# Kernel optimization log

Hardware: AMD Instinct MI355X
Metric: run time of the kernel (lower is better)

The kernel has to match this reference:

```python
import jax, jax.numpy as jnp
import numpy as np

B, N, D, NH, L, DFF = 2, 2048, 256, 8, 4, 1024
DH = D // NH
FACTOR = 0.5 / float(np.sqrt(DH))  # == 1/sqrt(4*DH), matches q/k feature dim 4*d_head
EPS = 1e-5


def _ln(x, g, b):
    m = x.mean(-1, keepdims=True)
    v = ((x - m) ** 2).mean(-1, keepdims=True)
    return (x - m) * jax.lax.rsqrt(v + EPS) * g + b


def setup_inputs() -> dict:
    key = jax.random.key(0)
    ks = jax.random.split(key, 16)
    s = 0.05
    r = lambda i, shape: jax.random.normal(ks[i], shape, dtype=jnp.float32)
    return {
        "H": r(0, (B, N, D)),
        "V": r(1, (B, N, 3, D)),
        "D_batch": r(2, (B, N, N)),
        "rbf_feat": r(3, (L, B, 1, N, N)),
        "H_mask": jnp.ones((B, N), dtype=bool),
        "ln1_g": jnp.ones((L, D)), "ln1_b": jnp.zeros((L, D)),
        "ln2_g": jnp.ones((L, D)), "ln2_b": jnp.zeros((L, D)),
        "Wq": r(4, (L, D, 4 * D)) * s, "bq": jnp.zeros((L, 4 * D)),
        "Wk": r(5, (L, D, 4 * D)) * s, "bk": jnp.zeros((L, 4 * D)),
        "Wv": r(6, (L, D, D)) * s, "bv": jnp.zeros((L, D)),
        "Wvv": r(7, (L, D, D)) * s,
        "Wo": r(8, (L, D, D)) * s, "bo": jnp.zeros((L, D)),
        "Wvo": r(9, (L, D, D)) * s,
        "Wlv": r(10, (L, D, 2 * D)) * s,
        "W1": r(11, (L, 2 * D, DFF)) * s, "b1": jnp.zeros((L, DFF)),
        "W2": r(12, (L, DFF, 2 * D)) * s, "b2": jnp.zeros((L, 2 * D)),
    }


def _stack_forward(H, V, D_batch, rbf_feat, H_mask, ln1_g, ln1_b, ln2_g, ln2_b,
                   Wq, bq, Wk, bk, Wv, bv, Wvv, Wo, bo, Wvo, Wlv, W1, b1, W2, b2):
    b, n = H.shape[:2]
    mask = H_mask[:, None, None, :]       # [B,1,1,N] masks key columns
    base_bias = D_batch[:, None]          # [B,1,N,N]

    def step(carry, xs):
        H, V = carry
        (rbf, g1, be1, g2, be2, wq, bq_, wk, bk_, wv, bv_, wvv,
         wo, bo_, wvo, wlv, w1, b1_, w2, b2_) = xs
        # --- self-attention sublayer (pre-LN on scalar stream only) ---
        Hn = _ln(H, g1, be1)
        Hq = (Hn @ wq + bq_).reshape(b, n, NH, 4 * DH)
        Hk = (Hn @ wk + bk_).reshape(b, n, NH, 4 * DH)
        Hv = (Hn @ wv + bv_).reshape(b, n, NH, DH)
        Vv = (V @ wvv).reshape(b, n, 3, NH, DH)
        Vv = jnp.swapaxes(Vv, 2, 3).reshape(b, n, NH, 3 * DH)
        V_attn = jnp.concatenate([Hv, Vv], axis=-1)        # [B,N,H,4*DH]
        bias = jnp.where(mask, rbf + base_bias, -jnp.inf)  # [B,1,N,N]
        scores = jnp.einsum('bnhd,bmhd->bhnm', Hq, Hk) * FACTOR + bias
        attn = jax.nn.softmax(scores, axis=-1)
        res = jnp.einsum('bhnm,bmhd->bnhd', attn, V_attn)  # [B,N,H,4*DH]
        H_res = res[..., :DH].reshape(b, n, D)
        V_res = jnp.swapaxes(res[..., DH:].reshape(b, n, NH, 3, DH), 2, 3).reshape(b, n, 3, D)
        H = H + (H_res @ wo + bo_)
        V = V + V_res @ wvo
        # --- GVP FFN sublayer (pre-LN on scalar stream only) ---
        Hn = _ln(H, g2, be2)
        Vp = V @ wlv                                       # [B,N,3,2D]
        V1, V2 = Vp[..., :D], Vp[..., D:]
        scaler = jnp.concatenate([Hn, jnp.linalg.norm(V1, axis=-2)], axis=-1)
        sc = jax.nn.silu(scaler @ w1 + b1_) @ w2 + b2_
        H = H + sc[..., :D]
        V = V + sc[..., D:][..., None, :] * V2             # vector_act='none'
        return (H, V), None

    xs = (rbf_feat, ln1_g, ln1_b, ln2_g, ln2_b, Wq, bq, Wk, bk, Wv, bv, Wvv,
          Wo, bo, Wvo, Wlv, W1, b1, W2, b2)
    (H, V), _ = jax.lax.scan(step, (H, V), xs)
    return H, V


def reference(H, V, D_batch, rbf_feat, H_mask, ln1_g, ln1_b, ln2_g, ln2_b,
              Wq, bq, Wk, bk, Wv, bv, Wvv, Wo, bo, Wvo, Wlv, W1, b1, W2, b2):
    return _stack_forward(H, V, D_batch, rbf_feat, H_mask, ln1_g, ln1_b, ln2_g, ln2_b,
                          Wq, bq, Wk, bk, Wv, bv, Wvv, Wo, bo, Wvo, Wlv, W1, b1, W2, b2)
```

## Files before the change

### kernel.cpp

```cpp
#include <hip/hip_runtime.h>
#include <math.h>

static constexpr int B_  = 2;
static constexpr int N_  = 2048;
static constexpr int D_  = 256;
static constexpr int NH_ = 8;
static constexpr int L_  = 4;
static constexpr int DH_ = 32;
static constexpr int DQ_ = 128;
static constexpr float FACTOR_ = 0.08838834764831845f;
static constexpr float LOG2E_  = 1.4426950408889634f;
static constexpr float EPS_ = 1e-5f;

typedef short    short8   __attribute__((ext_vector_type(8)));
typedef unsigned short us4 __attribute__((ext_vector_type(4)));
typedef unsigned short us8 __attribute__((ext_vector_type(8)));
typedef float    f32x4    __attribute__((ext_vector_type(4)));
typedef unsigned short us;

__device__ __forceinline__ us f2b(float f) {
  unsigned u = __float_as_uint(f);
  unsigned r = u + 0x7FFF + ((u >> 16) & 1);
  return (us)(r >> 16);
}
__device__ __forceinline__ float b2f(us u) {
  return __uint_as_float(((unsigned)u) << 16);
}
__device__ __forceinline__ float e2(float x) {
  return __builtin_amdgcn_exp2f(x);
}
__device__ __forceinline__ void gl_lds16(const void* g, void* l) {
  __builtin_amdgcn_global_load_lds(
      (const __attribute__((address_space(1))) void*)g,
      (__attribute__((address_space(3))) void*)l, 16, 0, 0);
}

__global__ __launch_bounds__(256) void ln_kernel(const float* __restrict__ X,
    const float* __restrict__ g, const float* __restrict__ b,
    us* __restrict__ Y) {
  __shared__ float r1[256], r2[256];
  int row = blockIdx.x, tid = threadIdx.x;
  float x = X[(size_t)row * D_ + tid];
  r1[tid] = x; r2[tid] = x * x;
  __syncthreads();
  for (int s = 128; s > 0; s >>= 1) {
    if (tid < s) { r1[tid] += r1[tid + s]; r2[tid] += r2[tid + s]; }
    __syncthreads();
  }
  float mean = r1[0] * (1.0f / D_);
  float var  = r2[0] * (1.0f / D_) - mean * mean;
  float inv  = rsqrtf(var + EPS_);
  Y[(size_t)row * D_ + tid] = f2b((x - mean) * inv * g[tid] + b[tid]);
}

__global__ __launch_bounds__(256) void conv_bf16(const float* __restrict__ X,
    us* __restrict__ Y) {
  size_t i = ((size_t)blockIdx.x * 256 + threadIdx.x) * 4;
  float4 v = *(const float4*)&X[i];
  us4 o = { f2b(v.x), f2b(v.y), f2b(v.z), f2b(v.w) };
  *(us4*)&Y[i] = o;
}

__global__ __launch_bounds__(256) void biascomb(const float* __restrict__ R,
    const float* __restrict__ Dq, us* __restrict__ Out) {
  size_t i = ((size_t)blockIdx.x * 256 + threadIdx.x) * 8;
  float4 r0 = *(const float4*)&R[i];
  float4 r1 = *(const float4*)&R[i + 4];
  float4 d0 = *(const float4*)&Dq[i];
  float4 d1 = *(const float4*)&Dq[i + 4];
  us8 o = { f2b((r0.x + d0.x) * LOG2E_), f2b((r0.y + d0.y) * LOG2E_),
            f2b((r0.z + d0.z) * LOG2E_), f2b((r0.w + d0.w) * LOG2E_),
            f2b((r1.x + d1.x) * LOG2E_), f2b((r1.y + d1.y) * LOG2E_),
            f2b((r1.z + d1.z) * LOG2E_), f2b((r1.w + d1.w) * LOG2E_) };
  *(us8*)&Out[i] = o;
}

struct WConvDesc {
  const float* src[9];
  unsigned dst[9];
  int K[9];
  int N[9];
  int start[10];
};
__global__ __launch_bounds__(256) void wconv_kernel(WConvDesc d, us* __restrict__ Wb) {
  __shared__ float T[64][65];
  int bid = blockIdx.x, tid = threadIdx.x;
  int j = 0;
  #pragma unroll
  for (int q = 0; q < 8; q++) if (bid >= d.start[q + 1]) j = q + 1;
  int t = bid - d.start[j];
  int K = d.K[j], N = d.N[j];
  int tpr = N >> 6;
  int tk = t / tpr, tn = t - tk * tpr;
  const float* src = d.src[j];
  us* dst = Wb + d.dst[j];
  #pragma unroll
  for (int i = 0; i < 4; i++) {
    int r = i * 16 + (tid >> 4), c = (tid & 15) * 4;
    *(float4*)&T[r][c] = *(const float4*)&src[(size_t)(tk * 64 + r) * N + tn * 64 + c];
  }
  __syncthreads();
  #pragma unroll
  for (int i = 0; i < 4; i++) {
    int n = i * 16 + (tid >> 4), k = (tid & 15) * 4;
    us4 o = { f2b(T[k][n]), f2b(T[k + 1][n]), f2b(T[k + 2][n]), f2b(T[k + 3][n]) };
    *(us4*)&dst[(size_t)(tn * 64 + n) * K + tk * 64 + k] = o;
  }
}

template<int BM, int BN, int BIAS, int ACC, int SILU, int WF, int WB, int QKV>
__global__ __launch_bounds__(256, 2) void gemm_v2(const us* __restrict__ A,
    const us* __restrict__ Wt, const float* __restrict__ bias,
    const float* __restrict__ bias2, const float* __restrict__ bias3,
    float* __restrict__ Cf, us* __restrict__ Cb,
    int M, int K, int Nc, float oscale) {
  constexpr int NFM = BM / 32, NFN = BN / 32;
  constexpr int WSM = NFM * 16, WSN = NFN * 16;
  constexpr int NLA = BM / 32, NLB = BN / 32;
  __shared__ us As[2][BM * 64];
  __shared__ us Bs[2][BN * 64];
  const int tid = threadIdx.x;
  const int w = tid >> 6, l = tid & 63;
  const int lx = l & 15, ly = l >> 4;
  const int wr = w >> 1, wc = w & 1;
  const int bn = blockIdx.x, bm = blockIdx.y;
  const int swz = (lx & 7) << 4;
  const char* Ag = (const char*)A + (size_t)(bm * BM) * K * 2;
  const char* Bg = (const char*)Wt + (size_t)(bn * BN) * K * 2;
  const size_t rowb = (size_t)K * 2;

  #define GSTAGE(buf, k0)                                                     \
    do {                                                                      \
      _Pragma("unroll")                                                       \
      for (int j = 0; j < NLA; j++) {                                         \
        int o = j * 4096 + tid * 16;                                          \
        int r = o >> 7, cb = o & 127;                                         \
        int sc = cb ^ ((r & 7) << 4);                                         \
        gl_lds16(Ag + (size_t)r * rowb + (size_t)(k0) * 2 + sc,               \
                 &As[buf][(j * 4096 + w * 1024) >> 1]);                       \
      }                                                                       \
      _Pragma("unroll")                                                       \
      for (int j = 0; j < NLB; j++) {                                         \
        int o = j * 4096 + tid * 16;                                          \
        int r = o >> 7, cb = o & 127;                                         \
        int sc = cb ^ ((r & 7) << 4);                                         \
        gl_lds16(Bg + (size_t)r * rowb + (size_t)(k0) * 2 + sc,               \
                 &Bs[buf][(j * 4096 + w * 1024) >> 1]);                       \
      }                                                                       \
    } while (0)

  f32x4 acc[NFM][NFN];
  #pragma unroll
  for (int i = 0; i < NFM; i++)
    #pragma unroll
    for (int j = 0; j < NFN; j++) acc[i][j] = (f32x4){0.f, 0.f, 0.f, 0.f};

  int cur = 0;
  GSTAGE(0, 0);
  __syncthreads();
  for (int k0 = 0; k0 < K; k0 += 64) {
    if (k0 + 64 < K) GSTAGE(cur ^ 1, k0 + 64);
    #pragma unroll
    for (int s = 0; s < 2; s++) {
      short8 af[NFM], bf[NFN];
      #pragma unroll
      for (int mt = 0; mt < NFM; mt++)
        af[mt] = *(const short8*)
            &As[cur][(((wr * WSM + mt * 16 + lx) * 128) + ((s * 64 + ly * 16) ^ swz)) >> 1];
      #pragma unroll
      for (int nt = 0; nt < NFN; nt++)
        bf[nt] = *(const short8*)
            &Bs[cur][(((wc * WSN + nt * 16 + lx) * 128) + ((s * 64 + ly * 16) ^ swz)) >> 1];
      __builtin_amdgcn_s_setprio(1);
      #pragma unroll
      for (int mt = 0; mt < NFM; mt++)
        #pragma unroll
        for (int nt = 0; nt < NFN; nt++)
          acc[mt][nt] = __builtin_amdgcn_mfma_f32_16x16x32_bf16(af[mt], bf[nt], acc[mt][nt], 0, 0, 0);
      __builtin_amdgcn_s_setprio(0);
    }
    __syncthreads();
    cur ^= 1;
  }
  #undef GSTAGE

  #pragma unroll
  for (int nt = 0; nt < NFN; nt++) {
    const int n = bn * BN + wc * WSN + nt * 16 + lx;
    float bval = 0.f, osc = oscale;
    if (QKV) {
      if (n < 1024)      { bval = bias[n]; }
      else if (n < 2048) { bval = bias2[n - 1024]; osc = 1.0f; }
      else               { bval = bias3[n - 2048]; osc = 1.0f; }
    } else if (BIAS) {
      bval = bias[n];
    }
    #pragma unroll
    for (int mt = 0; mt < NFM; mt++) {
      #pragma unroll
      for (int r = 0; r < 4; r++) {
        const int m = bm * BM + wr * WSM + mt * 16 + ly * 4 + r;
        float v = acc[mt][nt][r] + bval;
        if (SILU) v = v / (1.f + __expf(-v));
        size_t idx = (size_t)m * Nc + n;
        if (ACC) v += Cf[idx];
        if (WF) Cf[idx] = v;
        if (WB) Cb[idx] = f2b(v * osc);
      }
    }
  }
}

__global__ __launch_bounds__(256, 2) void gemm_wo(const us* __restrict__ Hres,
    const us* __restrict__ Vres, const us* __restrict__ WtO,
    const us* __restrict__ WtVO, const float* __restrict__ bo,
    float* __restrict__ Hs, float* __restrict__ Vs, us* __restrict__ Vb) {
  constexpr int K = 256, Nc = 256;
  __shared__ us As[2][64 * 64];
  __shared__ us Bs[2][64 * 64];
  const int tid = threadIdx.x;
  const int w = tid >> 6, l = tid & 63;
  const int lx = l & 15, ly = l >> 4;
  const int wr = w >> 1, wc = w & 1;
  const int bn = blockIdx.x, bm = blockIdx.y;
  const bool isH = bm < 64;
  const int mb = isH ? bm : bm - 64;
  const int swz = (lx & 7) << 4;
  const char* Ag = (const char*)(isH ? Hres : Vres) + (size_t)(mb * 64) * K * 2;
  const char* Bg = (const char*)(isH ? WtO : WtVO) + (size_t)(bn * 64) * K * 2;
  const size_t rowb = (size_t)K * 2;

  #define GSTAGE(buf, k0)                                                     \
    do {                                                                      \
      _Pragma("unroll")                                                       \
      for (int j = 0; j < 2; j++) {                                           \
        int o = j * 4096 + tid * 16;                                          \
        int r = o >> 7, cb = o & 127;                                         \
        int sc = cb ^ ((r & 7) << 4);                                         \
        gl_lds16(Ag + (size_t)r * rowb + (size_t)(k0) * 2 + sc,               \
                 &As[buf][(j * 4096 + w * 1024) >> 1]);                       \
        gl_lds16(Bg + (size_t)r * rowb + (size_t)(k0) * 2 + sc,               \
                 &Bs[buf][(j * 4096 + w * 1024) >> 1]);                       \
      }                                                                       \
    } while (0)

  f32x4 acc[2][2];
  #pragma unroll
  for (int i = 0; i < 2; i++)
    #pragma unroll
    for (int j = 0; j < 2; j++) acc[i][j] = (f32x4){0.f, 0.f, 0.f, 0.f};

  int cur = 0;
  GSTAGE(0, 0);
  __syncthreads();
  for (int k0 = 0; k0 < K; k0 += 64) {
    if (k0 + 64 < K) GSTAGE(cur ^ 1, k0 + 64);
    #pragma unroll
    for (int s = 0; s < 2; s++) {
      short8 af[2], bf[2];
      #pragma unroll
      for (int mt = 0; mt < 2; mt++)
        af[mt] = *(const short8*)
            &As[cur][(((wr * 32 + mt * 16 + lx) * 128) + ((s * 64 + ly * 16) ^ swz)) >> 1];
      #pragma unroll
      for (int nt = 0; nt < 2; nt++)
        bf[nt] = *(const short8*)
            &Bs[cur][(((wc * 32 + nt * 16 + lx) * 128) + ((s * 64 + ly * 16) ^ swz)) >> 1];
      __builtin_amdgcn_s_setprio(1);
      #pragma unroll
      for (int mt = 0; mt < 2; mt++)
        #pragma unroll
        for (int nt = 0; nt < 2; nt++)
          acc[mt][nt] = __builtin_amdgcn_mfma_f32_16x16x32_bf16(af[mt], bf[nt], acc[mt][nt], 0, 0, 0);
      __builtin_amdgcn_s_setprio(0);
    }
    __syncthreads();
    cur ^= 1;
  }
  #undef GSTAGE

  #pragma unroll
  for (int nt = 0; nt < 2; nt++) {
    const int n = bn * 64 + wc * 32 + nt * 16 + lx;
    const float bval = isH ? bo[n] : 0.f;
    #pragma unroll
    for (int mt = 0; mt < 2; mt++) {
      #pragma unroll
      for (int r = 0; r < 4; r++) {
        const int m = mb * 64 + wr * 32 + mt * 16 + ly * 4 + r;
        size_t idx = (size_t)m * Nc + n;
        float v = acc[mt][nt][r] + bval;
        if (isH) {
          Hs[idx] += v;
        } else {
          float nv = Vs[idx] + v;
          Vs[idx] = nv;
          Vb[idx] = f2b(nv);
        }
      }
    }
  }
}

__global__ __launch_bounds__(256, 2) void gemm_w2(const us* __restrict__ A,
    const us* __restrict__ Wt, const float* __restrict__ b2,
    const float* __restrict__ Vp, float* __restrict__ Hs,
    float* __restrict__ Vs, us* __restrict__ Vb) {
  constexpr int K = 1024;
  __shared__ us As[2][64 * 64];
  __shared__ us Bs[2][64 * 64];
  const int tid = threadIdx.x;
  const int w = tid >> 6, l = tid & 63;
  const int lx = l & 15, ly = l >> 4;
  const int wr = w >> 1, wc = w & 1;
  const int bn = blockIdx.x, bm = blockIdx.y;
  const int swz = (lx & 7) << 4;
  const char* Ag = (const char*)A + (size_t)(bm * 64) * K * 2;
  const char* Bg = (const char*)Wt + (size_t)(bn * 64) * K * 2;
  const size_t rowb = (size_t)K * 2;

  #define GSTAGE(buf, k0)                                                     \
    do {                                                                      \
      _Pragma("unroll")                                                       \
      for (int j = 0; j < 2; j++) {                                           \
        int o = j * 4096 + tid * 16;                                          \
        int r = o >> 7, cb = o & 127;                                         \
        int sc = cb ^ ((r & 7) << 4);                                         \
        gl_lds16(Ag + (size_t)r * rowb + (size_t)(k0) * 2 + sc,               \
                 &As[buf][(j * 4096 + w * 1024) >> 1]);                       \
        gl_lds16(Bg + (size_t)r * rowb + (size_t)(k0) * 2 + sc,               \
                 &Bs[buf][(j * 4096 + w * 1024) >> 1]);                       \
      }                                                                      \
    } while (0)

  f32x4 acc[2][2];
  #pragma unroll
  for (int i = 0; i < 2; i++)
    #pragma unroll
    for (int j = 0; j < 2; j++) acc[i][j] = (f32x4){0.f, 0.f, 0.f, 0.f};

  int cur = 0;
  GSTAGE(0, 0);
  __syncthreads();
  for (int k0 = 0; k0 < K; k0 += 64) {
    if (k0 + 64 < K) GSTAGE(cur ^ 1, k0 + 64);
    #pragma unroll
    for (int s = 0; s < 2; s++) {
      short8 af[2], bf[2];
      #pragma unroll
      for (int mt = 0; mt < 2; mt++)
        af[mt] = *(const short8*)
            &As[cur][(((wr * 32 + mt * 16 + lx) * 128) + ((s * 64 + ly * 16) ^ swz)) >> 1];
      #pragma unroll
      for (int nt = 0; nt < 2; nt++)
        bf[nt] = *(const short8*)
            &Bs[cur][(((wc * 32 + nt * 16 + lx) * 128) + ((s * 64 + ly * 16) ^ swz)) >> 1];
      __builtin_amdgcn_s_setprio(1);
      #pragma unroll
      for (int mt = 0; mt < 2; mt++)
        #pragma unroll
        for (int nt = 0; nt < 2; nt++)
          acc[mt][nt] = __builtin_amdgcn_mfma_f32_16x16x32_bf16(af[mt], bf[nt], acc[mt][nt], 0, 0, 0);
      __builtin_amdgcn_s_setprio(0);
    }
    __syncthreads();
    cur ^= 1;
  }
  #undef GSTAGE

  const bool isH = (bn < 4);
  #pragma unroll
  for (int nt = 0; nt < 2; nt++) {
    const int n = bn * 64 + wc * 32 + nt * 16 + lx;
    const float bval = b2[n];
    #pragma unroll
    for (int mt = 0; mt < 2; mt++) {
      #pragma unroll
      for (int r = 0; r < 4; r++) {
        const int m = bm * 64 + wr * 32 + mt * 16 + ly * 4 + r;
        float v = acc[mt][nt][r] + bval;
        if (isH) {
          Hs[(size_t)m * D_ + n] += v;
        } else {
          const int j = n - 256;
          #pragma unroll
          for (int c = 0; c < 3; c++) {
            size_t vi = ((size_t)m * 3 + c) * D_ + j;
            float nv = Vs[vi] + v * Vp[((size_t)m * 3 + c) * 512 + 256 + j];
            Vs[vi] = nv;
            Vb[vi] = f2b(nv);
          }
        }
      }
    }
  }
}

__global__ __launch_bounds__(256) void pack_vattn_t(const us* __restrict__ QKVb,
    const us* __restrict__ Vv, us* __restrict__ Vt) {
  __shared__ us T[64][136];
  const int bid = blockIdx.x;
  const int nt = bid & 31, hh = (bid >> 5) & 7, b = bid >> 8;
  const int n0 = nt * 64;
  const int tid = threadIdx.x;
  {
    const int nn = tid >> 2, part = tid & 3;
    const size_t row = (size_t)(b * N_ + n0 + nn);
    const us* src = (part == 0) ? (QKVb + row * 2304 + 2048 + hh * DH_)
                                : (Vv + (row * 3 + (part - 1)) * D_ + hh * DH_);
    #pragma unroll
    for (int jj = 0; jj < 32; jj += 8)
      *(us8*)&T[nn][part * 32 + jj] = *(const us8*)(src + jj);
  }
  __syncthreads();
  const int d = tid >> 1, half = tid & 1;
  size_t ob = ((size_t)(b * NH_ + hh) * DQ_ + d) * (size_t)N_ + n0 + half * 32;
  #pragma unroll
  for (int i = 0; i < 32; i += 8) {
    us8 o;
    #pragma unroll
    for (int e = 0; e < 8; e++) o[e] = T[half * 32 + i + e][d];
    *(us8*)&Vt[ob + i] = o;
  }
}

__global__ __launch_bounds__(256, 3) void attn_mfma(
    const us* __restrict__ QKVb,
    const us* __restrict__ Vtb,
    const us* __restrict__ bias,
    us* __restrict__ Hres,
    us* __restrict__ Vres) {
  __shared__ us Kt[8192];
  __shared__ us Vt[8192];
  __shared__ us Plds[4][16][72];
  const int bid = blockIdx.x;
  const int h  = bid >> 6;
  const int g  = bid & 63;
  const int b  = g >> 5;
  const int qt = g & 31;
  const int tid = threadIdx.x;
  const int w  = tid >> 6;
  const int l  = tid & 63;
  const int lx = l & 15;
  const int ly = l >> 4;
  const int qrow = qt * 64 + w * 16 + lx;
  const int swz = (lx & 7) << 4;

  short8 qf[4];
  {
    const us* qp = QKVb + (size_t)(b * N_ + qrow) * 2304 + h * DQ_ + ly * 8;
    #pragma unroll
    for (int s = 0; s < 4; s++) qf[s] = *(const short8*)(qp + s * 32);
  }
  const char* kg = (const char*)QKVb + (size_t)b * N_ * 4608 + 2048 + h * 256;
  const char* vg = (const char*)(Vtb + ((size_t)(b * NH_ + h) * DQ_) * (size_t)N_);
  const us* bbase = bias + ((size_t)b * N_ + qrow) * N_;

  us8 kreg[4], vreg[4];
  #define LOADKV(m0)                                                          \
    do {                                                                      \
      _Pragma("unroll")                                                       \
      for (int j = 0; j < 4; j++) {                                           \
        int o = j * 4096 + tid * 16;                                          \
        int rk = o >> 8, ck = o & 255;                                        \
        kreg[j] = *(const us8*)(kg + (size_t)((m0) + rk) * 4608 +             \
                                (ck ^ ((rk & 7) << 4)));                      \
        int rv = o >> 7, cv = o & 127;                                        \
        vreg[j] = *(const us8*)(vg + (size_t)rv * (N_ * 2) +                  \
                                (size_t)(m0) * 2 + (cv ^ ((rv & 7) << 4)));   \
      }                                                                       \
    } while (0)
  #define WRITEKV()                                                           \
    do {                                                                      \
      _Pragma("unroll")                                                       \
      for (int j = 0; j < 4; j++) {                                           \
        *(us8*)&Kt[j * 2048 + tid * 8] = kreg[j];                             \
        *(us8*)&Vt[j * 2048 + tid * 8] = vreg[j];                             \
      }                                                                       \
    } while (0)

  float m_run = -3.0e38f, l_run = 0.f;
  f32x4 oacc[8];
  #pragma unroll
  for (int i = 0; i < 8; i++) oacc[i] = (f32x4){0.f, 0.f, 0.f, 0.f};

  LOADKV(0);
  WRITEKV();
  LOADKV(64);
  us4 bb[4];
  #pragma unroll
  for (int t = 0; t < 4; t++) bb[t] = *(const us4*)(bbase + t * 16 + ly * 4);
  __syncthreads();

  for (int mc0 = 0; mc0 < N_; mc0 += 64) {
    us4 bbn[4];
    if (mc0 + 64 < N_) {
      #pragma unroll
      for (int t = 0; t < 4; t++)
        bbn[t] = *(const us4*)(bbase + mc0 + 64 + t * 16 + ly * 4);
    }
    f32x4 sacc[4];
    #pragma unroll
    for (int t = 0; t < 4; t++) sacc[t] = (f32x4){0.f, 0.f, 0.f, 0.f};
    __builtin_amdgcn_s_setprio(1);
    #pragma unroll
    for (int t = 0; t < 4; t++) {
      #pragma unroll
      for (int s = 0; s < 4; s++) {
        const short8 kf = *(const short8*)
            &Kt[((t * 16 + lx) * 256 + ((s * 64 + ly * 16) ^ swz)) >> 1];
        sacc[t] = __builtin_amdgcn_mfma_f32_16x16x32_bf16(kf, qf[s], sacc[t], 0, 0, 0);
      }
    }
    __builtin_amdgcn_s_setprio(0);
    float pvv[16];
    #pragma unroll
    for (int t = 0; t < 4; t++) {
      pvv[t*4+0] = sacc[t][0] + b2f(bb[t][0]);
      pvv[t*4+1] = sacc[t][1] + b2f(bb[t][1]);
      pvv[t*4+2] = sacc[t][2] + b2f(bb[t][2]);
      pvv[t*4+3] = sacc[t][3] + b2f(bb[t][3]);
    }
    float a8[8], a4[4];
    #pragma unroll
    for (int i = 0; i < 8; i++) a8[i] = fmaxf(pvv[i], pvv[i + 8]);
    #pragma unroll
    for (int i = 0; i < 4; i++) a4[i] = fmaxf(a8[i], a8[i + 4]);
    float mloc = fmaxf(fmaxf(a4[0], a4[1]), fmaxf(a4[2], a4[3]));
    if (!__all(mloc - m_run <= 11.54f)) {
      mloc = fmaxf(mloc, __shfl_xor(mloc, 16, 64));
      mloc = fmaxf(mloc, __shfl_xor(mloc, 32, 64));
      float m_new = fmaxf(m_run, mloc);
      float scale = e2(m_run - m_new);
      l_run *= scale;
      #pragma unroll
      for (int i = 0; i < 8; i++) {
        oacc[i][0] *= scale; oacc[i][1] *= scale;
        oacc[i][2] *= scale; oacc[i][3] *= scale;
      }
      m_run = m_new;
    }
    float s8[8], s4[4];
    #pragma unroll
    for (int i = 0; i < 16; i++) pvv[i] = e2(pvv[i] - m_run);
    #pragma unroll
    for (int i = 0; i < 8; i++) s8[i] = pvv[i] + pvv[i + 8];
    #pragma unroll
    for (int i = 0; i < 4; i++) s4[i] = s8[i] + s8[i + 4];
    l_run += (s4[0] + s4[1]) + (s4[2] + s4[3]);
    #pragma unroll
    for (int t = 0; t < 4; t++) {
      us4 pk = { f2b(pvv[t*4+0]), f2b(pvv[t*4+1]), f2b(pvv[t*4+2]), f2b(pvv[t*4+3]) };
      *(us4*)&Plds[w][lx][t * 16 + ly * 4] = pk;
    }
    short8 pf0 = *(const short8*)&Plds[w][lx][ly * 8];
    short8 pf1 = *(const short8*)&Plds[w][lx][32 + ly * 8];
    __builtin_amdgcn_s_setprio(1);
    #pragma unroll
    for (int dt = 0; dt < 8; dt++) {
      const int rb = (dt * 16 + lx) * 128;
      const short8 vf0 = *(const short8*)&Vt[(rb + ((ly * 16) ^ swz)) >> 1];
      const short8 vf1 = *(const short8*)&Vt[(rb + ((64 + ly * 16) ^ swz)) >> 1];
      oacc[dt] = __builtin_amdgcn_mfma_f32_16x16x32_bf16(vf0, pf0, oacc[dt], 0, 0, 0);
      oacc[dt] = __builtin_amdgcn_mfma_f32_16x16x32_bf16(vf1, pf1, oacc[dt], 0, 0, 0);
    }
    __builtin_amdgcn_s_setprio(0);
    __syncthreads();
    if (mc0 + 64 < N_) {
      WRITEKV();
      if (mc0 + 128 < N_) LOADKV(mc0 + 128);
      #pragma unroll
      for (int t = 0; t < 4; t++) bb[t] = bbn[t];
      __syncthreads();
    }
  }
  #undef LOADKV
  #undef WRITEKV
  l_run += __shfl_xor(l_run, 16, 64);
  l_run += __shfl_xor(l_run, 32, 64);
  float inv = 1.0f / l_run;
  const size_t row = (size_t)(b * N_ + qrow);
  #pragma unroll
  for (int dt = 0; dt < 8; dt++) {
    const int d0 = dt * 16 + ly * 4;
    us4 pk = { f2b(oacc[dt][0] * inv), f2b(oacc[dt][1] * inv),
               f2b(oacc[dt][2] * inv), f2b(oacc[dt][3] * inv) };
    if (d0 < 32) {
      *(us4*)&Hres[row * D_ + h * DH_ + d0] = pk;
    } else {
      const int c = (d0 - DH_) >> 5, dd = (d0 - DH_) & 31;
      *(us4*)&Vres[(row * 3 + c) * D_ + h * DH_ + dd] = pk;
    }
  }
}

__global__ __launch_bounds__(256) void ln2scaler(const float* __restrict__ H,
    const float* __restrict__ g, const float* __restrict__ b,
    const float* __restrict__ Vp, us* __restrict__ scal) {
  __shared__ float r1[256], r2[256];
  size_t row = blockIdx.x;
  int j = threadIdx.x;
  float x = H[row * D_ + j];
  r1[j] = x; r2[j] = x * x;
  __syncthreads();
  for (int s = 128; s > 0; s >>= 1) {
    if (j < s) { r1[j] += r1[j + s]; r2[j] += r2[j + s]; }
    __syncthreads();
  }
  float mean = r1[0] * (1.0f / D_);
  float var  = r2[0] * (1.0f / D_) - mean * mean;
  float inv  = rsqrtf(var + EPS_);
  scal[row * 512 + j] = f2b((x - mean) * inv * g[j] + b[j]);
  float a  = Vp[(row * 3 + 0) * 512 + j];
  float c1 = Vp[(row * 3 + 1) * 512 + j];
  float c2 = Vp[(row * 3 + 2) * 512 + j];
  scal[row * 512 + D_ + j] = f2b(sqrtf(a * a + c1 * c1 + c2 * c2));
}

extern "C" void kernel_launch(void* const* d_in, const int* in_sizes, int n_in,
                              void* d_out, int out_size, void* d_ws, size_t ws_size,
                              hipStream_t stream) {
  const float* H_in = (const float*)d_in[0];
  const float* V_in = (const float*)d_in[1];
  const float* Db   = (const float*)d_in[2];
  const float* rbf  = (const float*)d_in[3];
  const float* ln1g = (const float*)d_in[5];
  const float* ln1b = (const float*)d_in[6];
  const float* ln2g = (const float*)d_in[7];
  const float* ln2b = (const float*)d_in[8];
  const float* Wq  = (const float*)d_in[9];
  const float* bq  = (const float*)d_in[10];
  const float* Wk  = (const float*)d_in[11];
  const float* bk  = (const float*)d_in[12];
  const float* Wv  = (const float*)d_in[13];
  const float* bv  = (const float*)d_in[14];
  const float* Wvv = (const float*)d_in[15];
  const float* Wo  = (const float*)d_in[16];
  const float* bo  = (const float*)d_in[17];
  const float* Wvo = (const float*)d_in[18];
  const float* Wlv = (const float*)d_in[19];
  const float* W1  = (const float*)d_in[20];
  const float* b1  = (const float*)d_in[21];
  const float* W2  = (const float*)d_in[22];
  const float* b2  = (const float*)d_in[23];

  const size_t HN = (size_t)B_ * N_ * D_;
  const size_t VN = HN * 3;
  float* Hs = (float*)d_out;
  float* Vs = (float*)d_out + HN;
  float* ws = (float*)d_ws;
  us*    bias_b = (us*)ws;
  us*    Wb     = (us*)(ws + 4194304);
  us*    Vb     = (us*)(ws + 5177344);
  us*    Hnb    = (us*)(ws + 6750208);
  us*    QKVb   = (us*)(ws + 7274496);
  us*    Vtb    = (us*)(ws + 11993088);
  us*    Vvb    = (us*)(ws + 14090240);
  us*    Hres_b = (us*)(ws + 6750208);
  us*    Vres_b = (us*)(ws + 14090240);
  float* Vp     = ws + 7274496;
  us*    scal_b = (us*)(ws + 13565952);
  us*    midb   = (us*)(ws + 15014528);

  hipMemcpyAsync(Hs, H_in, HN * sizeof(float), hipMemcpyDeviceToDevice, stream);
  hipMemcpyAsync(Vs, V_in, VN * sizeof(float), hipMemcpyDeviceToDevice, stream);
  conv_bf16<<<3072, 256, 0, stream>>>(V_in, Vb);

  const int ROWS  = B_ * N_;
  static const int wKs[9] = {256,256,256,256,256,256,256,512,1024};
  static const int wNs[9] = {1024,1024,256,256,256,256,512,1024,512};
  static const unsigned wOff[9] = {0,262144,524288,589824,655360,720896,786432,917504,1441792};
  static const int wStart[10] = {0,64,128,144,160,176,192,224,352,480};

  for (int l = 0; l < L_; ++l) {
    WConvDesc dsc;
    const float* srcs[9] = {
      Wq  + (size_t)l * 256 * 1024, Wk  + (size_t)l * 256 * 1024,
      Wv  + (size_t)l * 256 * 256,  Wvv + (size_t)l * 256 * 256,
      Wo  + (size_t)l * 256 * 256,  Wvo + (size_t)l * 256 * 256,
      Wlv + (size_t)l * 256 * 512,  W1  + (size_t)l * 512 * 1024,
      W2  + (size_t)l * 1024 * 512 };
    for (int j = 0; j < 9; j++) {
      dsc.src[j] = srcs[j]; dsc.dst[j] = wOff[j];
      dsc.K[j] = wKs[j]; dsc.N[j] = wNs[j]; dsc.start[j] = wStart[j];
    }
    dsc.start[9] = wStart[9];
    wconv_kernel<<<480, 256, 0, stream>>>(dsc, Wb);
    biascomb<<<4096, 256, 0, stream>>>(rbf + (size_t)l * B_ * N_ * N_, Db, bias_b);
    if (l == 0)
      ln_kernel<<<ROWS, 256, 0, stream>>>(Hs, ln1g, ln1b, Hnb);

    gemm_v2<128,128,0,0,0,0,1,1><<<dim3(18, 32), 256, 0, stream>>>(
        Hnb, Wb + wOff[0], bq + l * 1024, bk + l * 1024, bv + l * 256,
        nullptr, QKVb, 4096, 256, 2304, FACTOR_ * LOG2E_);
    gemm_v2<64,64,0,0,0,0,1,0><<<dim3(4, 192), 256, 0, stream>>>(
        Vb, Wb + wOff[3], nullptr, nullptr, nullptr, nullptr, Vvb, 12288, 256, 256, 1.f);
    pack_vattn_t<<<512, 256, 0, stream>>>(QKVb, Vvb, Vtb);
    attn_mfma<<<512, 256, 0, stream>>>(QKVb, Vtb, bias_b, Hres_b, Vres_b);
    gemm_wo<<<dim3(4, 256), 256, 0, stream>>>(
        Hres_b, Vres_b, Wb + wOff[4], Wb + wOff[5], bo + l * 256, Hs, Vs, Vb);
    gemm_v2<64,64,0,0,0,1,0,0><<<dim3(8, 192), 256, 0, stream>>>(
        Vb, Wb + wOff[6], nullptr, nullptr, nullptr, Vp, nullptr, 12288, 256, 512, 1.f);
    ln2scaler<<<ROWS, 256, 0, stream>>>(Hs, ln2g + l * D_, ln2b + l * D_, Vp, scal_b);
    gemm_v2<128,64,1,0,1,0,1,0><<<dim3(16, 32), 256, 0, stream>>>(
        scal_b, Wb + wOff[7], b1 + l * 1024, nullptr, nullptr, nullptr, midb, 4096, 512, 1024, 1.f);
    gemm_w2<<<dim3(8, 64), 256, 0, stream>>>(
        midb, Wb + wOff[8], b2 + l * 512, Vp, Hs, Vs, Vb);
    if (l < 3)
      ln_kernel<<<ROWS, 256, 0, stream>>>(Hs, ln1g + (l + 1) * D_,
                                          ln1b + (l + 1) * D_, Hnb);
  }
}
```

Before: 785.9 us.

## Double attention key tile to 128 and store Vp intermediate in bf16

The attention kernel now processes 128 keys per iteration instead of 64. This doubles the K/V LDS tiles, the bias prefetch and the P staging buffer (now XOR-swizzled), and lowers launch bounds from 3 to 2 blocks per SM. The aim is to halve the per-tile sync and softmax-reduction overhead at the cost of occupancy and register pressure. Separately, the Wlv projection output Vp is written as bf16 rather than fp32, which halves its write and read traffic in ln2scaler and gemm_w2 but lowers the precision of the V2 multiplier and the vector norm.

```diff
diff --git a/kernel.cpp b/kernel.cpp
--- a/kernel.cpp
+++ b/kernel.cpp
@@ -304,7 +304,7 @@
 
 __global__ __launch_bounds__(256, 2) void gemm_w2(const us* __restrict__ A,
     const us* __restrict__ Wt, const float* __restrict__ b2,
-    const float* __restrict__ Vp, float* __restrict__ Hs,
+    const us* __restrict__ Vp, float* __restrict__ Hs,
     float* __restrict__ Vs, us* __restrict__ Vb) {
   constexpr int K = 1024;
   __shared__ us As[2][64 * 64];
@@ -386,7 +386,7 @@
           #pragma unroll
           for (int c = 0; c < 3; c++) {
             size_t vi = ((size_t)m * 3 + c) * D_ + j;
-            float nv = Vs[vi] + v * Vp[((size_t)m * 3 + c) * 512 + 256 + j];
+            float nv = Vs[vi] + v * b2f(Vp[((size_t)m * 3 + c) * 512 + 256 + j]);
             Vs[vi] = nv;
             Vb[vi] = f2b(nv);
           }
@@ -424,15 +424,15 @@
   }
 }
 
-__global__ __launch_bounds__(256, 3) void attn_mfma(
+__global__ __launch_bounds__(256, 2) void attn_mfma(
     const us* __restrict__ QKVb,
     const us* __restrict__ Vtb,
     const us* __restrict__ bias,
     us* __restrict__ Hres,
     us* __restrict__ Vres) {
-  __shared__ us Kt[8192];
-  __shared__ us Vt[8192];
-  __shared__ us Plds[4][16][72];
+  __shared__ us Kt[16384];
+  __shared__ us Vt[16384];
+  __shared__ us Plds[4][2048];
   const int bid = blockIdx.x;
   const int h  = bid >> 6;
   const int g  = bid & 63;
@@ -456,24 +456,23 @@
   const char* vg = (const char*)(Vtb + ((size_t)(b * NH_ + h) * DQ_) * (size_t)N_);
   const us* bbase = bias + ((size_t)b * N_ + qrow) * N_;
 
-  us8 kreg[4], vreg[4];
+  us8 kreg[8], vreg[8];
   #define LOADKV(m0)                                                          \
     do {                                                                      \
       _Pragma("unroll")                                                       \
-      for (int j = 0; j < 4; j++) {                                           \
+      for (int j = 0; j < 8; j++) {                                           \
         int o = j * 4096 + tid * 16;                                          \
         int rk = o >> 8, ck = o & 255;                                        \
         kreg[j] = *(const us8*)(kg + (size_t)((m0) + rk) * 4608 +             \
                                 (ck ^ ((rk & 7) << 4)));                      \
-        int rv = o >> 7, cv = o & 127;                                        \
-        vreg[j] = *(const us8*)(vg + (size_t)rv * (N_ * 2) +                  \
-                                (size_t)(m0) * 2 + (cv ^ ((rv & 7) << 4)));   \
+        vreg[j] = *(const us8*)(vg + (size_t)rk * (N_ * 2) +                  \
+                                (size_t)(m0) * 2 + (ck ^ ((rk & 7) << 4)));   \
       }                                                                       \
     } while (0)
   #define WRITEKV()                                                           \
     do {                                                                      \
       _Pragma("unroll")                                                       \
-      for (int j = 0; j < 4; j++) {                                           \
+      for (int j = 0; j < 8; j++) {                                           \
         *(us8*)&Kt[j * 2048 + tid * 8] = kreg[j];                             \
         *(us8*)&Vt[j * 2048 + tid * 8] = vreg[j];                             \
       }                                                                       \
@@ -486,25 +485,25 @@
 
   LOADKV(0);
   WRITEKV();
-  LOADKV(64);
-  us4 bb[4];
-  #pragma unroll
-  for (int t = 0; t < 4; t++) bb[t] = *(const us4*)(bbase + t * 16 + ly * 4);
+  LOADKV(128);
+  us4 bb[8];
+  #pragma unroll
+  for (int t = 0; t < 8; t++) bb[t] = *(const us4*)(bbase + t * 16 + ly * 4);
   __syncthreads();
 
-  for (int mc0 = 0; mc0 < N_; mc0 += 64) {
-    us4 bbn[4];
-    if (mc0 + 64 < N_) {
-      #pragma unroll
-      for (int t = 0; t < 4; t++)
-        bbn[t] = *(const us4*)(bbase + mc0 + 64 + t * 16 + ly * 4);
-    }
-    f32x4 sacc[4];
-    #pragma unroll
-    for (int t = 0; t < 4; t++) sacc[t] = (f32x4){0.f, 0.f, 0.f, 0.f};
+  for (int mc0 = 0; mc0 < N_; mc0 += 128) {
+    us4 bbn[8];
+    if (mc0 + 128 < N_) {
+      #pragma unroll
+      for (int t = 0; t < 8; t++)
+        bbn[t] = *(const us4*)(bbase + mc0 + 128 + t * 16 + ly * 4);
+    }
+    f32x4 sacc[8];
+    #pragma unroll
+    for (int t = 0; t < 8; t++) sacc[t] = (f32x4){0.f, 0.f, 0.f, 0.f};
     __builtin_amdgcn_s_setprio(1);
     #pragma unroll
-    for (int t = 0; t < 4; t++) {
+    for (int t = 0; t < 8; t++) {
       #pragma unroll
       for (int s = 0; s < 4; s++) {
         const short8 kf = *(const short8*)
@@ -513,17 +512,19 @@
       }
     }
     __builtin_amdgcn_s_setprio(0);
-    float pvv[16];
-    #pragma unroll
-    for (int t = 0; t < 4; t++) {
+    float pvv[32];
+    #pragma unroll
+    for (int t = 0; t < 8; t++) {
       pvv[t*4+0] = sacc[t][0] + b2f(bb[t][0]);
       pvv[t*4+1] = sacc[t][1] + b2f(bb[t][1]);
       pvv[t*4+2] = sacc[t][2] + b2f(bb[t][2]);
       pvv[t*4+3] = sacc[t][3] + b2f(bb[t][3]);
     }
-    float a8[8], a4[4];
-    #pragma unroll
-    for (int i = 0; i < 8; i++) a8[i] = fmaxf(pvv[i], pvv[i + 8]);
+    float a16[16], a8[8], a4[4];
+    #pragma unroll
+    for (int i = 0; i < 16; i++) a16[i] = fmaxf(pvv[i], pvv[i + 16]);
+    #pragma unroll
+    for (int i = 0; i < 8; i++) a8[i] = fmaxf(a16[i], a16[i + 8]);
     #pragma unroll
     for (int i = 0; i < 4; i++) a4[i] = fmaxf(a8[i], a8[i + 4]);
     float mloc = fmaxf(fmaxf(a4[0], a4[1]), fmaxf(a4[2], a4[3]));
@@ -540,37 +541,46 @@
       }
       m_run = m_new;
     }
-    float s8[8], s4[4];
-    #pragma unroll
-    for (int i = 0; i < 16; i++) pvv[i] = e2(pvv[i] - m_run);
-    #pragma unroll
-    for (int i = 0; i < 8; i++) s8[i] = pvv[i] + pvv[i + 8];
-    #pragma unroll
-    for (int i = 0; i < 4; i++) s4[i] = s8[i] + s8[i + 4];
-    l_run += (s4[0] + s4[1]) + (s4[2] + s4[3]);
-    #pragma unroll
-    for (int t = 0; t < 4; t++) {
+    #pragma unroll
+    for (int i = 0; i < 32; i++) pvv[i] = e2(pvv[i] - m_run);
+    {
+      float s16[16], s8v[8], s4v[4];
+      #pragma unroll
+      for (int i = 0; i < 16; i++) s16[i] = pvv[i] + pvv[i + 16];
+      #pragma unroll
+      for (int i = 0; i < 8; i++) s8v[i] = s16[i] + s16[i + 8];
+      #pragma unroll
+      for (int i = 0; i < 4; i++) s4v[i] = s8v[i] + s8v[i + 4];
+      l_run += (s4v[0] + s4v[1]) + (s4v[2] + s4v[3]);
+    }
+    #pragma unroll
+    for (int t = 0; t < 8; t++) {
       us4 pk = { f2b(pvv[t*4+0]), f2b(pvv[t*4+1]), f2b(pvv[t*4+2]), f2b(pvv[t*4+3]) };
-      *(us4*)&Plds[w][lx][t * 16 + ly * 4] = pk;
-    }
-    short8 pf0 = *(const short8*)&Plds[w][lx][ly * 8];
-    short8 pf1 = *(const short8*)&Plds[w][lx][32 + ly * 8];
+      *(us4*)((char*)&Plds[w][0] + lx * 256 + ((t * 32 + ly * 8) ^ swz)) = pk;
+    }
+    short8 pf[4];
+    #pragma unroll
+    for (int ks = 0; ks < 4; ks++)
+      pf[ks] = *(const short8*)((const char*)&Plds[w][0] + lx * 256 +
+                                ((ks * 64 + ly * 16) ^ swz));
     __builtin_amdgcn_s_setprio(1);
     #pragma unroll
     for (int dt = 0; dt < 8; dt++) {
-      const int rb = (dt * 16 + lx) * 128;
-      const short8 vf0 = *(const short8*)&Vt[(rb + ((ly * 16) ^ swz)) >> 1];
-      const short8 vf1 = *(const short8*)&Vt[(rb + ((64 + ly * 16) ^ swz)) >> 1];
-      oacc[dt] = __builtin_amdgcn_mfma_f32_16x16x32_bf16(vf0, pf0, oacc[dt], 0, 0, 0);
-      oacc[dt] = __builtin_amdgcn_mfma_f32_16x16x32_bf16(vf1, pf1, oacc[dt], 0, 0, 0);
+      const int rb = (dt * 16 + lx) * 256;
+      #pragma unroll
+      for (int ks = 0; ks < 4; ks++) {
+        const short8 vf = *(const short8*)
+            &Vt[(rb + ((ks * 64 + ly * 16) ^ swz)) >> 1];
+        oacc[dt] = __builtin_amdgcn_mfma_f32_16x16x32_bf16(vf, pf[ks], oacc[dt], 0, 0, 0);
+      }
     }
     __builtin_amdgcn_s_setprio(0);
     __syncthreads();
-    if (mc0 + 64 < N_) {
+    if (mc0 + 128 < N_) {
       WRITEKV();
-      if (mc0 + 128 < N_) LOADKV(mc0 + 128);
-      #pragma unroll
-      for (int t = 0; t < 4; t++) bb[t] = bbn[t];
+      if (mc0 + 256 < N_) LOADKV(mc0 + 256);
+      #pragma unroll
+      for (int t = 0; t < 8; t++) bb[t] = bbn[t];
       __syncthreads();
     }
   }
@@ -596,7 +606,7 @@
 
 __global__ __launch_bounds__(256) void ln2scaler(const float* __restrict__ H,
     const float* __restrict__ g, const float* __restrict__ b,
-    const float* __restrict__ Vp, us* __restrict__ scal) {
+    const us* __restrict__ Vp, us* __restrict__ scal) {
   __shared__ float r1[256], r2[256];
   size_t row = blockIdx.x;
   int j = threadIdx.x;
@@ -611,9 +621,9 @@
   float var  = r2[0] * (1.0f / D_) - mean * mean;
   float inv  = rsqrtf(var + EPS_);
   scal[row * 512 + j] = f2b((x - mean) * inv * g[j] + b[j]);
-  float a  = Vp[(row * 3 + 0) * 512 + j];
-  float c1 = Vp[(row * 3 + 1) * 512 + j];
-  float c2 = Vp[(row * 3 + 2) * 512 + j];
+  float a  = b2f(Vp[(row * 3 + 0) * 512 + j]);
+  float c1 = b2f(Vp[(row * 3 + 1) * 512 + j]);
+  float c2 = b2f(Vp[(row * 3 + 2) * 512 + j]);
   scal[row * 512 + D_ + j] = f2b(sqrtf(a * a + c1 * c1 + c2 * c2));
 }
 
@@ -658,7 +668,7 @@
   us*    Vvb    = (us*)(ws + 14090240);
   us*    Hres_b = (us*)(ws + 6750208);
   us*    Vres_b = (us*)(ws + 14090240);
-  float* Vp     = ws + 7274496;
+  us*    Vpb    = (us*)(ws + 7274496);
   us*    scal_b = (us*)(ws + 13565952);
   us*    midb   = (us*)(ws + 15014528);
 
@@ -699,13 +709,13 @@
     attn_mfma<<<512, 256, 0, stream>>>(QKVb, Vtb, bias_b, Hres_b, Vres_b);
     gemm_wo<<<dim3(4, 256), 256, 0, stream>>>(
         Hres_b, Vres_b, Wb + wOff[4], Wb + wOff[5], bo + l * 256, Hs, Vs, Vb);
-    gemm_v2<64,64,0,0,0,1,0,0><<<dim3(8, 192), 256, 0, stream>>>(
-        Vb, Wb + wOff[6], nullptr, nullptr, nullptr, Vp, nullptr, 12288, 256, 512, 1.f);
-    ln2scaler<<<ROWS, 256, 0, stream>>>(Hs, ln2g + l * D_, ln2b + l * D_, Vp, scal_b);
+    gemm_v2<64,64,0,0,0,0,1,0><<<dim3(8, 192), 256, 0, stream>>>(
+        Vb, Wb + wOff[6], nullptr, nullptr, nullptr, nullptr, Vpb, 12288, 256, 512, 1.f);
+    ln2scaler<<<ROWS, 256, 0, stream>>>(Hs, ln2g + l * D_, ln2b + l * D_, Vpb, scal_b);
     gemm_v2<128,64,1,0,1,0,1,0><<<dim3(16, 32), 256, 0, stream>>>(
         scal_b, Wb + wOff[7], b1 + l * 1024, nullptr, nullptr, nullptr, midb, 4096, 512, 1024, 1.f);
     gemm_w2<<<dim3(8, 64), 256, 0, stream>>>(
-        midb, Wb + wOff[8], b2 + l * 512, Vp, Hs, Vs, Vb);
+        midb, Wb + wOff[8], b2 + l * 512, Vpb, Hs, Vs, Vb);
     if (l < 3)
       ln_kernel<<<ROWS, 256, 0, stream>>>(Hs, ln1g + (l + 1) * D_,
                                           ln1b + (l + 1) * D_, Hnb);
```

Result: slower. 819.7 us (+4.3%).
